# Optimization experiments

Hardware: AMD Instinct MI355X
Metric: run time of the kernel (lower is better)

Reference implementation:

```python
import jax, jax.numpy as jnp
import numpy as np

B = 65536      # total rows = env_batch(8192) * n_slave(8)
DIN = 256      # input_shape
H = 64         # slave_hidden_dim
A = 32         # attention_dim
NACT = 14      # n_actions
NS = 8         # n_slave


def setup_inputs() -> dict:
    key = jax.random.key(0)
    ks = jax.random.split(key, 12)
    s = 0.05
    return {
        "obs": jax.random.normal(ks[0], (B, DIN), jnp.float32),
        "hidden_state": jax.random.normal(ks[1], (B, H), jnp.float32),
        "enc_W": jax.random.normal(ks[2], (DIN, H), jnp.float32) * s,
        "enc_b": jnp.zeros((H,), jnp.float32),
        "gru_Wih": jax.random.normal(ks[3], (3 * H, H), jnp.float32) * s,
        "gru_Whh": jax.random.normal(ks[4], (3 * H, H), jnp.float32) * s,
        "gru_bih": jnp.zeros((3 * H,), jnp.float32),
        "gru_bhh": jnp.zeros((3 * H,), jnp.float32),
        "qW": jax.random.normal(ks[5], (H, A), jnp.float32) * s,
        "kW": jax.random.normal(ks[6], (H, A), jnp.float32) * s,
        "vW": jax.random.normal(ks[7], (H, A), jnp.float32) * s,
        "vb": jnp.zeros((A,), jnp.float32),
        "decW": jax.random.normal(ks[8], (H + A, NACT), jnp.float32) * s,
        "decb": jnp.zeros((NACT,), jnp.float32),
        "n_slave": NS,
    }


def reference(obs, hidden_state, enc_W, enc_b, gru_Wih, gru_Whh, gru_bih, gru_bhh,
              qW, kW, vW, vb, decW, decb, n_slave):
    # encoding + ReLU
    x = jax.nn.relu(obs @ enc_W + enc_b)                      # [B, H]
    # torch GRUCell: r,z,n gate order in weight rows
    gx = x @ gru_Wih.T + gru_bih                              # [B, 3H]
    gh = hidden_state @ gru_Whh.T + gru_bhh                   # [B, 3H]
    xr, xz, xn = jnp.split(gx, 3, axis=-1)
    hr, hz, hn = jnp.split(gh, 3, axis=-1)
    r = jax.nn.sigmoid(xr + hr)
    z = jax.nn.sigmoid(xz + hz)
    n = jnp.tanh(xn + r * hn)
    h_out = (1.0 - z) * n + z * hidden_state                  # [B, H]

    Ad = qW.shape[-1]
    q = (h_out @ qW).reshape(-1, n_slave, Ad)                 # [b, n, A]
    k = (h_out @ kW).reshape(-1, n_slave, Ad)
    v = jax.nn.relu(h_out @ vW + vb).reshape(-1, n_slave, Ad)

    # exclude-self attention == diagonal-masked softmax attention
    scores = jnp.einsum('bia,bja->bij', q, k) / jnp.sqrt(jnp.float32(Ad))
    eye = jnp.eye(n_slave, dtype=bool)
    scores = jnp.where(eye, jnp.float32(-1e9), scores)
    attn = jax.nn.softmax(scores, axis=-1)                    # [b, n, n]
    xatt = jnp.einsum('bij,bja->bia', attn, v).reshape(-1, Ad)  # [B, A]

    out = jnp.concatenate([h_out, xatt], axis=-1) @ decW + decb  # [B, n_actions]
    return (out, h_out)
```

## Files before the change

kernel.cpp:

```cpp
#include <hip/hip_runtime.h>


#define NACT 14
#define BTOT 65536

typedef unsigned int  u32;
typedef unsigned short u16;
using short8 = __attribute__((ext_vector_type(8))) short;
using f32x4  = __attribute__((ext_vector_type(4))) float;

#define ENC0 0
#define WIH0 16384
#define WHH0 28672
#define QKV0 40960
#define DEC0 47104
#define WTOT 48640

__device__ u16   g_wbuf[WTOT];
__device__ float g_bias[256];

__device__ __forceinline__ u32 f2bf_rne(float f){
  u32 x = __float_as_uint(f);
  return (x + 0x7fffu + ((x >> 16) & 1u)) >> 16;
}
__device__ __forceinline__ u32 pk2(float a, float b){
  u32 d;
  asm("v_cvt_pk_bf16_f32 %0, %1, %2" : "=v"(d) : "v"(a), "v"(b));
  return d;
}
__device__ __forceinline__ float blo(u32 u){ return __uint_as_float(u << 16); }
__device__ __forceinline__ float bhi(u32 u){ return __uint_as_float(u & 0xffff0000u); }
__device__ __forceinline__ float sigm(float x){ return 1.0f / (1.0f + __expf(-x)); }
__device__ __forceinline__ float tanhp(float x){ return 1.0f - 2.0f / (__expf(2.0f * x) + 1.0f); }
__device__ __forceinline__ short8 as_s8(uint4 v){ union { uint4 u; short8 s; } x; x.u = v; return x.s; }

#define MFMA16(a,b,c) __builtin_amdgcn_mfma_f32_16x16x32_bf16((a),(b),(c),0,0,0)

__global__ void prep(const float* __restrict__ encW, const float* __restrict__ Wih,
                     const float* __restrict__ Whh,  const float* __restrict__ qW,
                     const float* __restrict__ kW,   const float* __restrict__ vW,
                     const float* __restrict__ decW, const float* __restrict__ bih,
                     const float* __restrict__ bhh)
{
  int j = blockIdx.x * 256 + threadIdx.x;
  if (blockIdx.x == 0) {
    int n = threadIdx.x & 63, g = threadIdx.x >> 6;
    float v;
    if      (g == 0) v = bih[n]       + bhh[n];
    else if (g == 1) v = bih[64 + n]  + bhh[64 + n];
    else if (g == 2) v = bih[128 + n];
    else             v = bhh[128 + n];
    g_bias[threadIdx.x] = v;
  }
  if (j >= WTOT) return;
  int pos  = j & 511;
  int lane = pos >> 3, jj = pos & 7;
  int quad = lane >> 4, l16 = lane & 15;
  float val = 0.f;
  if (j < WIH0) {
    int f = j >> 9, ks = f >> 2, t = f & 3;
    int k = ks * 32 + quad * 8 + jj, n = 16 * t + l16;
    val = encW[k * 64 + n];
  } else if (j < WHH0) {
    int f = (j - WIH0) >> 9;
    int u = f / 6, g = (f >> 1) % 3, ks = f & 1;
    int wrow = 64 * g + 16 * u + l16, k = ks * 32 + quad * 8 + jj;
    val = Wih[wrow * 64 + k];
  } else if (j < QKV0) {
    int f = (j - WHH0) >> 9;
    int u = f / 6, g = (f >> 1) % 3, ks = f & 1;
    int wrow = 64 * g + 16 * u + l16, k = ks * 32 + quad * 8 + jj;
    val = Whh[wrow * 64 + k];
  } else if (j < DEC0) {
    int f = (j - QKV0) >> 9, t = f >> 1, ks = f & 1;
    int n = 16 * t + l16, mtx = n >> 5, nn = n & 31;
    int k = ks * 32 + quad * 8 + jj;
    val = (mtx == 0) ? qW[k * 32 + nn] * 0.17677669529663687f
        : (mtx == 1) ? kW[k * 32 + nn] : vW[k * 32 + nn];
  } else {
    int f = (j - DEC0) >> 9;
    int k = f * 32 + quad * 8 + jj, n = l16;
    if (n < 14) val = decW[k * 14 + n];
  }
  g_wbuf[j] = (u16)f2bf_rne(val);
}

__global__ __launch_bounds__(128, 2)
void commslave_main(const float* __restrict__ obs,  const float* __restrict__ hid,
                    const float* __restrict__ encb, const float* __restrict__ vb,
                    const float* __restrict__ decb, float* __restrict__ out)
{
  __shared__ __align__(16) u16 ldsU[17920];

  const int tid  = threadIdx.x;
  const int lane = tid & 63;
  const int w    = tid >> 6;
  const int quad = lane >> 4;
  const int l16  = lane & 15;
  const int M0   = 32 * w;
  const int gr   = blockIdx.x * 64 + M0;
  float* Sf = (float*)(ldsU + 9216) + w * (32 * 68);

  #pragma unroll
  for (int i = 0; i < 8; i++) {
    int c = lane + 64 * i;
    int lr = c >> 4, c4 = c & 15;
    float4 v = ((const float4*)hid)[(size_t)(gr + lr) * 16 + c4];
    *(uint2*)&ldsU[4608 + (M0 + lr) * 72 + c4 * 4] = make_uint2(pk2(v.x, v.y), pk2(v.z, v.w));
  }

  f32x4 ce[2][4];
  #pragma unroll
  for (int t = 0; t < 4; t++) {
    float bv = encb[16 * t + l16];
    ce[0][t] = (f32x4){bv, bv, bv, bv};
    ce[1][t] = (f32x4){bv, bv, bv, bv};
  }
  #pragma unroll
  for (int ks = 0; ks < 8; ks++) {
    short8 a[2];
    #pragma unroll
    for (int mt = 0; mt < 2; mt++) {
      const float* ap = obs + (size_t)(gr + 16 * mt + l16) * 256 + ks * 32 + quad * 8;
      float4 a0 = *(const float4*)ap, a1 = *(const float4*)(ap + 4);
      a[mt] = as_s8(make_uint4(pk2(a0.x, a0.y), pk2(a0.z, a0.w), pk2(a1.x, a1.y), pk2(a1.z, a1.w)));
    }
    #pragma unroll
    for (int t = 0; t < 4; t++) {
      short8 b = as_s8(*(const uint4*)&g_wbuf[ENC0 + (ks * 4 + t) * 512 + lane * 8]);
      ce[0][t] = MFMA16(a[0], b, ce[0][t]);
      ce[1][t] = MFMA16(a[1], b, ce[1][t]);
    }
  }
  #pragma unroll
  for (int mt = 0; mt < 2; mt++)
    #pragma unroll
    for (int t = 0; t < 4; t++)
      #pragma unroll
      for (int r = 0; r < 4; r++)
        Sf[(16 * mt + quad * 4 + r) * 68 + 16 * t + l16] = fmaxf(ce[mt][t][r], 0.f);
  #pragma unroll
  for (int i = 0; i < 4; i++) {
    int c = lane + 64 * i, lr = c >> 3, j = c & 7;
    const float* sp = &Sf[lr * 68 + 8 * j];
    float4 v0 = *(const float4*)sp, v1 = *(const float4*)(sp + 4);
    *(uint4*)&ldsU[(M0 + lr) * 72 + 8 * j] =
        make_uint4(pk2(v0.x, v0.y), pk2(v0.z, v0.w), pk2(v1.x, v1.y), pk2(v1.z, v1.w));
  }
  __syncthreads();

  short8 ax[2][2], ah[2][2];
  #pragma unroll
  for (int mt = 0; mt < 2; mt++)
    #pragma unroll
    for (int ks = 0; ks < 2; ks++) {
      ax[mt][ks] = *(const short8*)&ldsU[(M0 + 16 * mt + l16) * 72 + ks * 32 + quad * 8];
      ah[mt][ks] = *(const short8*)&ldsU[4608 + (M0 + 16 * mt + l16) * 72 + ks * 32 + quad * 8];
    }
  #pragma unroll 1
  for (int u = 0; u < 4; u++) {
    f32x4 g6[2][6];
    #pragma unroll
    for (int mt = 0; mt < 2; mt++)
      #pragma unroll
      for (int t = 0; t < 6; t++) g6[mt][t] = (f32x4){0.f, 0.f, 0.f, 0.f};
    #pragma unroll
    for (int g = 0; g < 3; g++) {
      #pragma unroll
      for (int ks = 0; ks < 2; ks++) {
        int f = (u * 3 + g) * 2 + ks;
        short8 bi = as_s8(*(const uint4*)&g_wbuf[WIH0 + f * 512 + lane * 8]);
        short8 bh = as_s8(*(const uint4*)&g_wbuf[WHH0 + f * 512 + lane * 8]);
        #pragma unroll
        for (int mt = 0; mt < 2; mt++) {
          g6[mt][g]     = MFMA16(ax[mt][ks], bi, g6[mt][g]);
          g6[mt][3 + g] = MFMA16(ah[mt][ks], bh, g6[mt][3 + g]);
        }
      }
    }
    int nc = 16 * u + l16;
    float brz = g_bias[nc], bzz = g_bias[64 + nc], bni = g_bias[128 + nc], bnh = g_bias[192 + nc];
    #pragma unroll
    for (int mt = 0; mt < 2; mt++)
      #pragma unroll
      for (int r = 0; r < 4; r++) {
        int lr = 16 * mt + quad * 4 + r;
        float hp = blo(ldsU[4608 + (M0 + lr) * 72 + nc]);
        float rg = sigm(g6[mt][0][r] + g6[mt][3][r] + brz);
        float zg = sigm(g6[mt][1][r] + g6[mt][4][r] + bzz);
        float nn = tanhp(g6[mt][2][r] + bni + rg * (g6[mt][5][r] + bnh));
        Sf[lr * 68 + nc] = (1.f - zg) * nn + zg * hp;
      }
  }
  #pragma unroll
  for (int i = 0; i < 4; i++) {
    int c = lane + 64 * i, lr = c >> 3, j = c & 7;
    const float* sp = &Sf[lr * 68 + 8 * j];
    float4 v0 = *(const float4*)sp, v1 = *(const float4*)(sp + 4);
    *(uint4*)&ldsU[4608 + (M0 + lr) * 72 + 8 * j] =
        make_uint4(pk2(v0.x, v0.y), pk2(v0.z, v0.w), pk2(v1.x, v1.y), pk2(v1.z, v1.w));
  }
  __syncthreads();

  short8 hx[2][2];
  #pragma unroll
  for (int mt = 0; mt < 2; mt++)
    #pragma unroll
    for (int ks = 0; ks < 2; ks++)
      hx[mt][ks] = *(const short8*)&ldsU[4608 + (M0 + 16 * mt + l16) * 72 + ks * 32 + quad * 8];
  f32x4 cq[2][6];
  #pragma unroll
  for (int t = 0; t < 6; t++) {
    float bv = (t >= 4) ? vb[16 * (t - 4) + l16] : 0.f;
    cq[0][t] = (f32x4){bv, bv, bv, bv};
    cq[1][t] = (f32x4){bv, bv, bv, bv};
  }
  #pragma unroll
  for (int ks = 0; ks < 2; ks++)
    #pragma unroll
    for (int t = 0; t < 6; t++) {
      short8 b = as_s8(*(const uint4*)&g_wbuf[QKV0 + (t * 2 + ks) * 512 + lane * 8]);
      cq[0][t] = MFMA16(hx[0][ks], b, cq[0][t]);
      cq[1][t] = MFMA16(hx[1][ks], b, cq[1][t]);
    }
  #pragma unroll
  for (int mt = 0; mt < 2; mt++) {
    #pragma unroll
    for (int t = 0; t < 4; t++)
      #pragma unroll
      for (int r = 0; r < 4; r++)
        Sf[(16 * mt + quad * 4 + r) * 68 + 16 * t + l16] = cq[mt][t][r];
    #pragma unroll
    for (int t = 4; t < 6; t++)
      #pragma unroll
      for (int r = 0; r < 4; r++)
        ldsU[(M0 + 16 * mt + quad * 4 + r) * 72 + 32 + 16 * (t - 4) + l16] =
            (u16)pk2(fmaxf(cq[mt][t][r], 0.f), 0.f);
  }
  __syncthreads();

  {
    const int r_l = lane >> 1, s2 = lane & 1;
    const int gb = r_l & ~7, ri = r_l & 7;
    const float* fq = &Sf[r_l * 68];
    float sc[4];
    #pragma unroll
    for (int jj = 0; jj < 4; jj++) {
      int j = 4 * s2 + jj;
      const float* fk = &Sf[(gb + j) * 68 + 32];
      float d = 0.f;
      #pragma unroll
      for (int a4 = 0; a4 < 32; a4 += 4) {
        float4 q4 = *(const float4*)&fq[a4];
        float4 k4 = *(const float4*)&fk[a4];
        d += q4.x * k4.x + q4.y * k4.y + q4.z * k4.z + q4.w * k4.w;
      }
      sc[jj] = (j == ri) ? -1e30f : d;
    }
    float m = fmaxf(fmaxf(sc[0], sc[1]), fmaxf(sc[2], sc[3]));
    m = fmaxf(m, __shfl_xor(m, 1));
    float p[4], sum = 0.f;
    #pragma unroll
    for (int jj = 0; jj < 4; jj++) {
      int j = 4 * s2 + jj;
      p[jj] = (j == ri) ? 0.f : __expf(sc[jj] - m);
      sum += p[jj];
    }
    sum += __shfl_xor(sum, 1);
    float inv = 1.f / sum;
    #pragma unroll
    for (int jj = 0; jj < 4; jj++)
      Sf[r_l * 68 + 4 * s2 + jj] = p[jj] * inv;
    float xa[16];
    #pragma unroll
    for (int u = 0; u < 16; u++) xa[u] = 0.f;
    #pragma unroll
    for (int j = 0; j < 8; j++) {
      float aj = Sf[r_l * 68 + j];
      const u16* vp = &ldsU[(M0 + gb + j) * 72 + 32 + 16 * s2];
      uint4 v0 = *(const uint4*)vp, v1 = *(const uint4*)(vp + 8);
      xa[0]  += aj * blo(v0.x); xa[1]  += aj * bhi(v0.x);
      xa[2]  += aj * blo(v0.y); xa[3]  += aj * bhi(v0.y);
      xa[4]  += aj * blo(v0.z); xa[5]  += aj * bhi(v0.z);
      xa[6]  += aj * blo(v0.w); xa[7]  += aj * bhi(v0.w);
      xa[8]  += aj * blo(v1.x); xa[9]  += aj * bhi(v1.x);
      xa[10] += aj * blo(v1.y); xa[11] += aj * bhi(v1.y);
      xa[12] += aj * blo(v1.z); xa[13] += aj * bhi(v1.z);
      xa[14] += aj * blo(v1.w); xa[15] += aj * bhi(v1.w);
    }
    u16* xp = &ldsU[(M0 + r_l) * 72 + 16 * s2];
    *(uint4*)xp = make_uint4(pk2(xa[0], xa[1]), pk2(xa[2], xa[3]),
                             pk2(xa[4], xa[5]), pk2(xa[6], xa[7]));
    *(uint4*)(xp + 8) = make_uint4(pk2(xa[8], xa[9]),  pk2(xa[10], xa[11]),
                                   pk2(xa[12], xa[13]), pk2(xa[14], xa[15]));
  }
  __syncthreads();

  {
    float db = (l16 < NACT) ? decb[l16] : 0.f;
    f32x4 co[2] = {(f32x4){db, db, db, db}, (f32x4){db, db, db, db}};
    #pragma unroll
    for (int ks = 0; ks < 2; ks++) {
      short8 b = as_s8(*(const uint4*)&g_wbuf[DEC0 + ks * 512 + lane * 8]);
      #pragma unroll
      for (int mt = 0; mt < 2; mt++) {
        short8 a = *(const short8*)&ldsU[4608 + (M0 + 16 * mt + l16) * 72 + ks * 32 + quad * 8];
        co[mt] = MFMA16(a, b, co[mt]);
      }
    }
    short8 b2 = as_s8(*(const uint4*)&g_wbuf[DEC0 + 2 * 512 + lane * 8]);
    #pragma unroll
    for (int mt = 0; mt < 2; mt++) {
      short8 a2 = *(const short8*)&ldsU[(M0 + 16 * mt + l16) * 72 + quad * 8];
      co[mt] = MFMA16(a2, b2, co[mt]);
    }
    if (l16 < NACT)
      #pragma unroll
      for (int mt = 0; mt < 2; mt++)
        #pragma unroll
        for (int r = 0; r < 4; r++)
          out[(size_t)(gr + 16 * mt + quad * 4 + r) * NACT + l16] = co[mt][r];
  }

  {
    float* outH = out + (size_t)BTOT * NACT;
    #pragma unroll
    for (int i = 0; i < 4; i++) {
      int c = lane + 64 * i, lr = c >> 3, j = c & 7;
      uint4 u = *(const uint4*)&ldsU[4608 + (M0 + lr) * 72 + 8 * j];
      *(float4*)(outH + (size_t)(gr + lr) * 64 + 8 * j) =
          make_float4(blo(u.x), bhi(u.x), blo(u.y), bhi(u.y));
      *(float4*)(outH + (size_t)(gr + lr) * 64 + 8 * j + 4) =
          make_float4(blo(u.z), bhi(u.z), blo(u.w), bhi(u.w));
    }
  }
}

extern "C" void kernel_launch(void* const* d_in, const int* in_sizes, int n_in,
                              void* d_out, int out_size, void* d_ws, size_t ws_size,
                              hipStream_t stream) {
  (void)in_sizes; (void)n_in; (void)d_ws; (void)ws_size; (void)out_size;
  const float* obs  = (const float*)d_in[0];
  const float* hid  = (const float*)d_in[1];
  const float* encW = (const float*)d_in[2];
  const float* encb = (const float*)d_in[3];
  const float* Wih  = (const float*)d_in[4];
  const float* Whh  = (const float*)d_in[5];
  const float* bih  = (const float*)d_in[6];
  const float* bhh  = (const float*)d_in[7];
  const float* qW   = (const float*)d_in[8];
  const float* kW   = (const float*)d_in[9];
  const float* vW   = (const float*)d_in[10];
  const float* vb   = (const float*)d_in[11];
  const float* decW = (const float*)d_in[12];
  const float* decb = (const float*)d_in[13];
  float* out = (float*)d_out;

  prep<<<(WTOT + 255) / 256, 256, 0, stream>>>(encW, Wih, Whh, qW, kW, vW, decW, bih, bhh);
  commslave_main<<<BTOT / 64, 128, 0, stream>>>(obs, hid, encb, vb, decb, out);
}
```

Before: 151.3 us.

## Use single-wave blocks, drop barriers, and double-buffer obs loads

Each block now holds one 64-lane wavefront over 32 rows, so every __syncthreads and the fp32 staging round-trips through LDS go away: ReLU and GRU outputs are written straight to LDS as bf16. Obs tiles are prefetched two K-steps ahead into registers, and the hidden-state load is issued up front to overlap with the encoder MMA. The aim is to cut barrier stalls and LDS traffic and hide global-load latency, at the cost of more registers and twice as many blocks.

```diff
diff --git a/kernel.cpp b/kernel.cpp
--- a/kernel.cpp
+++ b/kernel.cpp
@@ -85,28 +85,39 @@
   g_wbuf[j] = (u16)f2bf_rne(val);
 }
 
-__global__ __launch_bounds__(128, 2)
+__global__ __launch_bounds__(64, 2)
 void commslave_main(const float* __restrict__ obs,  const float* __restrict__ hid,
                     const float* __restrict__ encb, const float* __restrict__ vb,
                     const float* __restrict__ decb, float* __restrict__ out)
 {
-  __shared__ __align__(16) u16 ldsU[17920];
-
-  const int tid  = threadIdx.x;
-  const int lane = tid & 63;
-  const int w    = tid >> 6;
+  __shared__ __align__(16) u16 ldsU[8960];
+
+  const int lane = threadIdx.x & 63;
   const int quad = lane >> 4;
   const int l16  = lane & 15;
-  const int M0   = 32 * w;
-  const int gr   = blockIdx.x * 64 + M0;
-  float* Sf = (float*)(ldsU + 9216) + w * (32 * 68);
+  const int gr   = blockIdx.x * 32;
+  float* Sf = (float*)(ldsU + 4608);
+
+  float4 hv[8];
+  #pragma unroll
+  for (int i = 0; i < 8; i++) {
+    int c = lane + 64 * i;
+    hv[i] = ((const float4*)hid)[(size_t)(gr + (c >> 4)) * 16 + (c & 15)];
+  }
+  float4 pre[2][2][2];
+  #pragma unroll
+  for (int mt = 0; mt < 2; mt++) {
+    const float* ap = obs + (size_t)(gr + 16 * mt + l16) * 256 + quad * 8;
+    pre[0][mt][0] = *(const float4*)ap;        pre[0][mt][1] = *(const float4*)(ap + 4);
+    pre[1][mt][0] = *(const float4*)(ap + 32); pre[1][mt][1] = *(const float4*)(ap + 36);
+  }
 
   #pragma unroll
   for (int i = 0; i < 8; i++) {
     int c = lane + 64 * i;
     int lr = c >> 4, c4 = c & 15;
-    float4 v = ((const float4*)hid)[(size_t)(gr + lr) * 16 + c4];
-    *(uint2*)&ldsU[4608 + (M0 + lr) * 72 + c4 * 4] = make_uint2(pk2(v.x, v.y), pk2(v.z, v.w));
+    *(uint2*)&ldsU[2304 + lr * 72 + c4 * 4] =
+        make_uint2(pk2(hv[i].x, hv[i].y), pk2(hv[i].z, hv[i].w));
   }
 
   f32x4 ce[2][4];
@@ -118,12 +129,20 @@
   }
   #pragma unroll
   for (int ks = 0; ks < 8; ks++) {
+    const int s = ks & 1;
     short8 a[2];
     #pragma unroll
     for (int mt = 0; mt < 2; mt++) {
-      const float* ap = obs + (size_t)(gr + 16 * mt + l16) * 256 + ks * 32 + quad * 8;
-      float4 a0 = *(const float4*)ap, a1 = *(const float4*)(ap + 4);
+      float4 a0 = pre[s][mt][0], a1 = pre[s][mt][1];
       a[mt] = as_s8(make_uint4(pk2(a0.x, a0.y), pk2(a0.z, a0.w), pk2(a1.x, a1.y), pk2(a1.z, a1.w)));
+    }
+    if (ks < 6) {
+      #pragma unroll
+      for (int mt = 0; mt < 2; mt++) {
+        const float* ap = obs + (size_t)(gr + 16 * mt + l16) * 256 + (ks + 2) * 32 + quad * 8;
+        pre[s][mt][0] = *(const float4*)ap;
+        pre[s][mt][1] = *(const float4*)(ap + 4);
+      }
     }
     #pragma unroll
     for (int t = 0; t < 4; t++) {
@@ -137,25 +156,18 @@
     #pragma unroll
     for (int t = 0; t < 4; t++)
       #pragma unroll
-      for (int r = 0; r < 4; r++)
-        Sf[(16 * mt + quad * 4 + r) * 68 + 16 * t + l16] = fmaxf(ce[mt][t][r], 0.f);
-  #pragma unroll
-  for (int i = 0; i < 4; i++) {
-    int c = lane + 64 * i, lr = c >> 3, j = c & 7;
-    const float* sp = &Sf[lr * 68 + 8 * j];
-    float4 v0 = *(const float4*)sp, v1 = *(const float4*)(sp + 4);
-    *(uint4*)&ldsU[(M0 + lr) * 72 + 8 * j] =
-        make_uint4(pk2(v0.x, v0.y), pk2(v0.z, v0.w), pk2(v1.x, v1.y), pk2(v1.z, v1.w));
-  }
-  __syncthreads();
+      for (int r = 0; r < 4; r++) {
+        float xv = fmaxf(ce[mt][t][r], 0.f);
+        ldsU[(16 * mt + quad * 4 + r) * 72 + 16 * t + l16] = (u16)pk2(xv, xv);
+      }
 
   short8 ax[2][2], ah[2][2];
   #pragma unroll
   for (int mt = 0; mt < 2; mt++)
     #pragma unroll
     for (int ks = 0; ks < 2; ks++) {
-      ax[mt][ks] = *(const short8*)&ldsU[(M0 + 16 * mt + l16) * 72 + ks * 32 + quad * 8];
-      ah[mt][ks] = *(const short8*)&ldsU[4608 + (M0 + 16 * mt + l16) * 72 + ks * 32 + quad * 8];
+      ax[mt][ks] = *(const short8*)&ldsU[(16 * mt + l16) * 72 + ks * 32 + quad * 8];
+      ah[mt][ks] = *(const short8*)&ldsU[2304 + (16 * mt + l16) * 72 + ks * 32 + quad * 8];
     }
   #pragma unroll 1
   for (int u = 0; u < 4; u++) {
@@ -180,34 +192,31 @@
     }
     int nc = 16 * u + l16;
     float brz = g_bias[nc], bzz = g_bias[64 + nc], bni = g_bias[128 + nc], bnh = g_bias[192 + nc];
+    float hp[2][4];
+    #pragma unroll
+    for (int mt = 0; mt < 2; mt++)
+      #pragma unroll
+      for (int r = 0; r < 4; r++)
+        hp[mt][r] = blo(ldsU[2304 + (16 * mt + quad * 4 + r) * 72 + nc]);
     #pragma unroll
     for (int mt = 0; mt < 2; mt++)
       #pragma unroll
       for (int r = 0; r < 4; r++) {
         int lr = 16 * mt + quad * 4 + r;
-        float hp = blo(ldsU[4608 + (M0 + lr) * 72 + nc]);
         float rg = sigm(g6[mt][0][r] + g6[mt][3][r] + brz);
         float zg = sigm(g6[mt][1][r] + g6[mt][4][r] + bzz);
         float nn = tanhp(g6[mt][2][r] + bni + rg * (g6[mt][5][r] + bnh));
-        Sf[lr * 68 + nc] = (1.f - zg) * nn + zg * hp;
-      }
-  }
-  #pragma unroll
-  for (int i = 0; i < 4; i++) {
-    int c = lane + 64 * i, lr = c >> 3, j = c & 7;
-    const float* sp = &Sf[lr * 68 + 8 * j];
-    float4 v0 = *(const float4*)sp, v1 = *(const float4*)(sp + 4);
-    *(uint4*)&ldsU[4608 + (M0 + lr) * 72 + 8 * j] =
-        make_uint4(pk2(v0.x, v0.y), pk2(v0.z, v0.w), pk2(v1.x, v1.y), pk2(v1.z, v1.w));
-  }
-  __syncthreads();
+        float ho = (1.f - zg) * nn + zg * hp[mt][r];
+        ldsU[2304 + lr * 72 + nc] = (u16)pk2(ho, ho);
+      }
+  }
 
   short8 hx[2][2];
   #pragma unroll
   for (int mt = 0; mt < 2; mt++)
     #pragma unroll
     for (int ks = 0; ks < 2; ks++)
-      hx[mt][ks] = *(const short8*)&ldsU[4608 + (M0 + 16 * mt + l16) * 72 + ks * 32 + quad * 8];
+      hx[mt][ks] = *(const short8*)&ldsU[2304 + (16 * mt + l16) * 72 + ks * 32 + quad * 8];
   f32x4 cq[2][6];
   #pragma unroll
   for (int t = 0; t < 6; t++) {
@@ -234,10 +243,9 @@
     for (int t = 4; t < 6; t++)
       #pragma unroll
       for (int r = 0; r < 4; r++)
-        ldsU[(M0 + 16 * mt + quad * 4 + r) * 72 + 32 + 16 * (t - 4) + l16] =
+        ldsU[(16 * mt + quad * 4 + r) * 72 + 32 + 16 * (t - 4) + l16] =
             (u16)pk2(fmaxf(cq[mt][t][r], 0.f), 0.f);
   }
-  __syncthreads();
 
   {
     const int r_l = lane >> 1, s2 = lane & 1;
@@ -277,7 +285,7 @@
     #pragma unroll
     for (int j = 0; j < 8; j++) {
       float aj = Sf[r_l * 68 + j];
-      const u16* vp = &ldsU[(M0 + gb + j) * 72 + 32 + 16 * s2];
+      const u16* vp = &ldsU[(gb + j) * 72 + 32 + 16 * s2];
       uint4 v0 = *(const uint4*)vp, v1 = *(const uint4*)(vp + 8);
       xa[0]  += aj * blo(v0.x); xa[1]  += aj * bhi(v0.x);
       xa[2]  += aj * blo(v0.y); xa[3]  += aj * bhi(v0.y);
@@ -288,13 +296,12 @@
       xa[12] += aj * blo(v1.z); xa[13] += aj * bhi(v1.z);
       xa[14] += aj * blo(v1.w); xa[15] += aj * bhi(v1.w);
     }
-    u16* xp = &ldsU[(M0 + r_l) * 72 + 16 * s2];
+    u16* xp = &ldsU[r_l * 72 + 16 * s2];
     *(uint4*)xp = make_uint4(pk2(xa[0], xa[1]), pk2(xa[2], xa[3]),
                              pk2(xa[4], xa[5]), pk2(xa[6], xa[7]));
     *(uint4*)(xp + 8) = make_uint4(pk2(xa[8], xa[9]),  pk2(xa[10], xa[11]),
                                    pk2(xa[12], xa[13]), pk2(xa[14], xa[15]));
   }
-  __syncthreads();
 
   {
     float db = (l16 < NACT) ? decb[l16] : 0.f;
@@ -304,14 +311,14 @@
       short8 b = as_s8(*(const uint4*)&g_wbuf[DEC0 + ks * 512 + lane * 8]);
       #pragma unroll
       for (int mt = 0; mt < 2; mt++) {
-        short8 a = *(const short8*)&ldsU[4608 + (M0 + 16 * mt + l16) * 72 + ks * 32 + quad * 8];
+        short8 a = *(const short8*)&ldsU[2304 + (16 * mt + l16) * 72 + ks * 32 + quad * 8];
         co[mt] = MFMA16(a, b, co[mt]);
       }
     }
     short8 b2 = as_s8(*(const uint4*)&g_wbuf[DEC0 + 2 * 512 + lane * 8]);
     #pragma unroll
     for (int mt = 0; mt < 2; mt++) {
-      short8 a2 = *(const short8*)&ldsU[(M0 + 16 * mt + l16) * 72 + quad * 8];
+      short8 a2 = *(const short8*)&ldsU[(16 * mt + l16) * 72 + quad * 8];
       co[mt] = MFMA16(a2, b2, co[mt]);
     }
     if (l16 < NACT)
@@ -327,7 +334,7 @@
     #pragma unroll
     for (int i = 0; i < 4; i++) {
       int c = lane + 64 * i, lr = c >> 3, j = c & 7;
-      uint4 u = *(const uint4*)&ldsU[4608 + (M0 + lr) * 72 + 8 * j];
+      uint4 u = *(const uint4*)&ldsU[2304 + lr * 72 + 8 * j];
       *(float4*)(outH + (size_t)(gr + lr) * 64 + 8 * j) =
           make_float4(blo(u.x), bhi(u.x), blo(u.y), bhi(u.y));
       *(float4*)(outH + (size_t)(gr + lr) * 64 + 8 * j + 4) =
@@ -357,5 +364,5 @@
   float* out = (float*)d_out;
 
   prep<<<(WTOT + 255) / 256, 256, 0, stream>>>(encW, Wih, Whh, qW, kW, vW, decW, bih, bhh);
-  commslave_main<<<BTOT / 64, 128, 0, stream>>>(obs, hid, encb, vb, decb, out);
-}
+  commslave_main<<<BTOT / 32, 64, 0, stream>>>(obs, hid, encb, vb, decb, out);
+}
```

Result: no change. 149.9 us (-0.9%).
